# Optimization experiments

Measured on AMD Instinct MI355X. Metric: run time of the kernel, lower is better.

The kernel has to match this reference:

```python
import jax, jax.numpy as jnp
import numpy as np

HID, H, D, DFF = 128, 4, 128, 2048   # hidden_dim, nheads, out_feats per head, dim_feedforward
N, E, B = 32768, 524288, 32
EPS = 1e-5
SLOPE = 0.2  # DGL EdgeGATConv negative_slope default


def setup_inputs() -> dict:
    key = jax.random.key(0)
    ks = jax.random.split(key, 16)
    s = 0.05
    return {
        "h": jax.random.normal(ks[0], (N, HID), jnp.float32),
        "e": jax.random.normal(ks[1], (E, 1), jnp.float32),
        "src": jax.random.randint(ks[2], (E,), 0, N, jnp.int32),
        "dst": jax.random.randint(ks[3], (E,), 0, N, jnp.int32),
        "batch_size": B,
        # EdgeGATConv params (fc / fc_edge / res_fc are bias-free in DGL)
        "W_fc": jax.random.normal(ks[4], (HID, H * D), jnp.float32) * s,
        "attn_l": jax.random.normal(ks[5], (H, D), jnp.float32) * s,
        "attn_r": jax.random.normal(ks[6], (H, D), jnp.float32) * s,
        "W_fe": jax.random.normal(ks[7], (1, H * D), jnp.float32) * s,
        "attn_e": jax.random.normal(ks[8], (H, D), jnp.float32) * s,
        "W_res": jax.random.normal(ks[9], (HID, H * D), jnp.float32) * s,
        "gat_bias": jnp.zeros((H * D,), jnp.float32),
        # linear_mha + norms + FFN
        "W_mha": jax.random.normal(ks[10], (H * D, HID), jnp.float32) * s,
        "b_mha": jnp.zeros((HID,), jnp.float32),
        "n1_g": jnp.ones((HID,), jnp.float32),
        "n1_b": jnp.zeros((HID,), jnp.float32),
        "n2_g": jnp.ones((HID,), jnp.float32),
        "n2_b": jnp.zeros((HID,), jnp.float32),
        "W1": jax.random.normal(ks[11], (HID, DFF), jnp.float32) * s,
        "b1": jnp.zeros((DFF,), jnp.float32),
        "W2": jax.random.normal(ks[12], (DFF, HID), jnp.float32) * s,
        "b2": jnp.zeros((HID,), jnp.float32),
    }


def _ln(x, g, b):
    mu = x.mean(-1, keepdims=True)
    var = ((x - mu) ** 2).mean(-1, keepdims=True)
    return (x - mu) * jax.lax.rsqrt(var + EPS) * g + b


def reference(h, e, src, dst, batch_size, W_fc, attn_l, attn_r, W_fe, attn_e,
              W_res, gat_bias, W_mha, b_mha, n1_g, n1_b, n2_g, n2_b,
              W1, b1, W2, b2):
    n = h.shape[0]
    h0 = h
    # --- EdgeGATConv (eval mode: dropouts are identity) ---
    ft = (h @ W_fc).reshape(n, H, D)                         # (N,H,D)
    el = jnp.einsum("nhd,hd->nh", ft, attn_l)                # (N,H)
    er = jnp.einsum("nhd,hd->nh", ft, attn_r)
    fe = (e @ W_fe).reshape(-1, H, D)                        # (E,H,D)
    ee = jnp.einsum("ehd,hd->eh", fe, attn_e)                # (E,H)
    sc = jax.nn.leaky_relu(el[src] + er[dst] + ee, SLOPE)    # (E,H)
    # segment softmax over incoming edges of each dst node
    m = jax.ops.segment_max(sc, dst, num_segments=n)         # (N,H)
    m = jnp.where(jnp.isfinite(m), m, 0.0)                   # empty segments
    w = jnp.exp(sc - m[dst])
    z = jax.ops.segment_sum(w, dst, num_segments=n)
    zd = z[dst]
    alpha = w / jnp.where(zd == 0, 1.0, zd)                  # (E,H)
    msg = ft[src] * alpha[:, :, None]                        # (E,H,D)
    rst = jax.ops.segment_sum(msg, dst, num_segments=n)      # (N,H,D)
    rst = rst + (h0 @ W_res).reshape(n, H, D) + gat_bias.reshape(1, H, D)
    # --- transformer wrapper ---
    x = jax.nn.relu(rst).reshape(n, H * D)
    x = jax.nn.relu(x @ W_mha + b_mha)
    x = _ln(h0 + x, n1_g, n1_b)
    x = x.reshape(batch_size, -1, x.shape[1])                # (B, N/B, HID)
    ff = jax.nn.relu(x @ W1 + b1) @ W2 + b2
    return _ln(x + ff, n2_g, n2_b)
```

## Files before the change

kernel.cpp:

```cpp
#include <hip/hip_runtime.h>
#include <hip/hip_bf16.h>

#define N_NODES 32768
#define E_EDGES 524288
#define HIDDIM 128
#define FDIM 512
#define DFF 2048
#define LN_EPS 1e-5f
#define SLOPE 0.2f
#define CAP 64

typedef __bf16 bf16_t;
typedef __bf16 bf16x8 __attribute__((ext_vector_type(8)));
typedef float f32x4 __attribute__((ext_vector_type(4)));
typedef float f32x2 __attribute__((ext_vector_type(2)));

#define GLD_LDS16(gp, lp) __builtin_amdgcn_global_load_lds( \
    (const __attribute__((address_space(1))) unsigned int*)(gp), \
    (__attribute__((address_space(3))) unsigned int*)(lp), 16, 0, 0)

__device__ inline unsigned char f32_to_e4m3(float v) {
#if __has_builtin(__builtin_amdgcn_cvt_pk_fp8_f32)
    return (unsigned char)(__builtin_amdgcn_cvt_pk_fp8_f32(v, v, 0, false) & 0xff);
#else
    unsigned bits = __float_as_uint(v);
    unsigned sign = (bits >> 24) & 0x80;
    float av = fabsf(v);
    if (av >= 448.f) return (unsigned char)(sign | 0x7E);
    int e = (int)((bits >> 23) & 0xFF) - 127;
    if (e < -6) { int n = (int)rintf(av * 512.f); return (unsigned char)(sign | n); }
    float ulp = exp2f((float)(e - 3));
    int n = (int)rintf(av / ulp);
    if (n == 16) { e += 1; n = 8; }
    return (unsigned char)(sign | ((e + 7) << 3) | (n - 8));
#endif
}
template<bool HI>
__device__ inline f32x2 e4m3x2_to_f32(unsigned u) {
#if __has_builtin(__builtin_amdgcn_cvt_pk_f32_fp8)
    return __builtin_amdgcn_cvt_pk_f32_fp8(u, HI);
#else
    f32x2 r;
    unsigned b0 = HI ? ((u >> 16) & 0xff) : (u & 0xff);
    unsigned b1 = HI ? ((u >> 24) & 0xff) : ((u >> 8) & 0xff);
    unsigned bs[2] = {b0, b1};
    for (int i = 0; i < 2; ++i) {
        unsigned b = bs[i];
        float s = (b & 0x80) ? -1.f : 1.f;
        int e = (b >> 3) & 15, m = b & 7;
        float v = e ? (8 + m) * exp2f((float)(e - 10)) : m * exp2f(-9.f);
        r[i] = s * v;
    }
    return r;
#endif
}

__device__ inline void pack_range(const float* __restrict__ B, bf16_t* __restrict__ out,
                                  int id, int N) {
    const int g = id / N, n = id % N;
    union { bf16_t b[8]; uint4 u; } pk;
#pragma unroll
    for (int j = 0; j < 8; ++j) pk.b[j] = (bf16_t)B[(size_t)(g * 8 + j) * N + n];
    *(uint4*)(out + (size_t)id * 8) = pk.u;
}

__global__ __launch_bounds__(256) void prep_kernel(const float* __restrict__ h, bf16_t* __restrict__ hb,
                                                   const float* __restrict__ W_fc, bf16_t* __restrict__ Wfc_p,
                                                   const float* __restrict__ W_res, bf16_t* __restrict__ Wres_p,
                                                   const float* __restrict__ W_mha, bf16_t* __restrict__ Wmha_p,
                                                   const float* __restrict__ W1, bf16_t* __restrict__ W1_p,
                                                   const float* __restrict__ W2, bf16_t* __restrict__ W2_p,
                                                   const float* __restrict__ W_fe, const float* __restrict__ attn_e,
                                                   float* __restrict__ ce) {
    int bid = blockIdx.x;
    const int tid = threadIdx.x;
    if (bid < 4096) {
        const int id = bid * 256 + tid;
        const float4 v = ((const float4*)h)[id];
        union { bf16_t b[4]; uint2 u; } pk;
        pk.b[0] = (bf16_t)v.x; pk.b[1] = (bf16_t)v.y; pk.b[2] = (bf16_t)v.z; pk.b[3] = (bf16_t)v.w;
        *(uint2*)(hb + (size_t)id * 4) = pk.u;
        return;
    }
    bid -= 4096;
    if (bid < 32)  { pack_range(W_fc,  Wfc_p,  bid * 256 + tid, 512);  return; }
    bid -= 32;
    if (bid < 32)  { pack_range(W_res, Wres_p, bid * 256 + tid, 512);  return; }
    bid -= 32;
    if (bid < 32)  { pack_range(W_mha, Wmha_p, bid * 256 + tid, 128);  return; }
    bid -= 32;
    if (bid < 128) { pack_range(W1,    W1_p,   bid * 256 + tid, 2048); return; }
    bid -= 128;
    if (bid < 128) { pack_range(W2,    W2_p,   bid * 256 + tid, 128);  return; }
    if (tid < 128) {
        const float4 w = ((const float4*)W_fe)[tid];
        const float4 a = ((const float4*)attn_e)[tid];
        float p = w.x * a.x + w.y * a.y + w.z * a.z + w.w * a.w;
        for (int off = 16; off; off >>= 1) p += __shfl_down(p, off, 32);
        if ((tid & 31) == 0) ce[tid >> 5] = p;
    }
}

__global__ __launch_bounds__(256) void gemm_mfma(const bf16_t* __restrict__ A,
                                                 const bf16_t* __restrict__ Bp,
                                                 bf16_t* __restrict__ C,
                                                 int M, int N, int K) {
    __shared__ __align__(16) bf16_t lA[4096];
    __shared__ __align__(16) bf16_t lB[4096];
    const int tid = threadIdx.x;
    const int lane = tid & 63;
    const int wave = tid >> 6;
    const int wm = (wave >> 1) * 64, wn = (wave & 1) * 64;
    const int row0 = blockIdx.y * 128, col0 = blockIdx.x * 128;
    const int ko = lane >> 4;
    const int rl = lane & 15;
    f32x4 acc[4][4] = {};
    const int c0 = tid, c1 = tid + 256;
    const int g0 = c0 >> 7, m0 = c0 & 127;
    const int g1 = c1 >> 7, m1 = c1 & 127;
    for (int k0 = 0; k0 < K; k0 += 32) {
        __syncthreads();
        GLD_LDS16(A + (size_t)(row0 + m0) * K + k0 + g0 * 8, lA + c0 * 8);
        GLD_LDS16(A + (size_t)(row0 + m1) * K + k0 + g1 * 8, lA + c1 * 8);
        GLD_LDS16(Bp + ((size_t)(k0 / 8 + g0) * N + col0 + m0) * 8, lB + c0 * 8);
        GLD_LDS16(Bp + ((size_t)(k0 / 8 + g1) * N + col0 + m1) * 8, lB + c1 * 8);
        __syncthreads();
        bf16x8 af[4], bfr[4];
#pragma unroll
        for (int i = 0; i < 4; ++i) {
            af[i]  = *(const bf16x8*)&lA[(ko * 128 + wm + i * 16 + rl) * 8];
            bfr[i] = *(const bf16x8*)&lB[(ko * 128 + wn + i * 16 + rl) * 8];
        }
#pragma unroll
        for (int i = 0; i < 4; ++i)
#pragma unroll
            for (int j = 0; j < 4; ++j)
                acc[i][j] = __builtin_amdgcn_mfma_f32_16x16x32_bf16(af[i], bfr[j], acc[i][j], 0, 0, 0);
    }
    const int cr = (lane >> 4) * 4;
    const int cc = lane & 15;
#pragma unroll
    for (int i = 0; i < 4; ++i)
#pragma unroll
        for (int j = 0; j < 4; ++j) {
            const int col = col0 + wn + j * 16 + cc;
#pragma unroll
            for (int r = 0; r < 4; ++r) {
                const int row = row0 + wm + i * 16 + cr + r;
                C[(size_t)row * N + col] = (bf16_t)acc[i][j][r];
            }
        }
}

__global__ __launch_bounds__(256) void gemm_ft(const bf16_t* __restrict__ A,
                                               const bf16_t* __restrict__ Bp,
                                               const float* __restrict__ attn_l,
                                               const float* __restrict__ attn_r,
                                               unsigned char* __restrict__ ft8,
                                               float* __restrict__ el,
                                               float* __restrict__ er) {
    __shared__ __align__(16) bf16_t lA[4096];
    __shared__ __align__(16) bf16_t lB[4096];
    __shared__ float s_el[2][128], s_er[2][128];
    const int tid = threadIdx.x, lane = tid & 63, wave = tid >> 6;
    const int wm = (wave >> 1) * 64, wn = (wave & 1) * 64;
    const int row0 = blockIdx.y * 128;
    const int head = blockIdx.x, col0 = head * 128;
    const int ko = lane >> 4, rl = lane & 15;
    f32x4 acc[4][4] = {};
    const int c0 = tid, c1 = tid + 256;
    const int g0 = c0 >> 7, m0 = c0 & 127;
    const int g1 = c1 >> 7, m1 = c1 & 127;
    for (int k0 = 0; k0 < 128; k0 += 32) {
        __syncthreads();
        GLD_LDS16(A + (size_t)(row0 + m0) * 128 + k0 + g0 * 8, lA + c0 * 8);
        GLD_LDS16(A + (size_t)(row0 + m1) * 128 + k0 + g1 * 8, lA + c1 * 8);
        GLD_LDS16(Bp + ((size_t)(k0 / 8 + g0) * 512 + col0 + m0) * 8, lB + c0 * 8);
        GLD_LDS16(Bp + ((size_t)(k0 / 8 + g1) * 512 + col0 + m1) * 8, lB + c1 * 8);
        __syncthreads();
        bf16x8 af[4], bfr[4];
#pragma unroll
        for (int i = 0; i < 4; ++i) {
            af[i]  = *(const bf16x8*)&lA[(ko * 128 + wm + i * 16 + rl) * 8];
            bfr[i] = *(const bf16x8*)&lB[(ko * 128 + wn + i * 16 + rl) * 8];
        }
#pragma unroll
        for (int i = 0; i < 4; ++i)
#pragma unroll
            for (int j = 0; j < 4; ++j)
                acc[i][j] = __builtin_amdgcn_mfma_f32_16x16x32_bf16(af[i], bfr[j], acc[i][j], 0, 0, 0);
    }
    const int cr = (lane >> 4) * 4, cc = lane & 15;
    float al[4], ar[4];
#pragma unroll
    for (int j = 0; j < 4; ++j) {
        al[j] = attn_l[col0 + wn + j * 16 + cc];
        ar[j] = attn_r[col0 + wn + j * 16 + cc];
    }
#pragma unroll
    for (int i = 0; i < 4; ++i)
#pragma unroll
        for (int r = 0; r < 4; ++r) {
            const int row = row0 + wm + i * 16 + cr + r;
            float pel = 0.f, per = 0.f;
#pragma unroll
            for (int j = 0; j < 4; ++j) {
                const float v = acc[i][j][r];
                ft8[(size_t)row * 512 + col0 + wn + j * 16 + cc] = f32_to_e4m3(v);
                pel += v * al[j];
                per += v * ar[j];
            }
#pragma unroll
            for (int m = 1; m < 16; m <<= 1) {
                pel += __shfl_xor(pel, m);
                per += __shfl_xor(per, m);
            }
            if (cc == 0) {
                s_el[wn >> 6][wm + i * 16 + cr + r] = pel;
                s_er[wn >> 6][wm + i * 16 + cr + r] = per;
            }
        }
    __syncthreads();
    if (tid < 128) {
        el[(size_t)(row0 + tid) * 4 + head] = s_el[0][tid] + s_el[1][tid];
        er[(size_t)(row0 + tid) * 4 + head] = s_er[0][tid] + s_er[1][tid];
    }
}

__global__ __launch_bounds__(256) void gemm_mha_ln(const bf16_t* __restrict__ A,
                                                   const bf16_t* __restrict__ Bp,
                                                   const float* __restrict__ bias,
                                                   const float* __restrict__ h0,
                                                   const float* __restrict__ gamma,
                                                   const float* __restrict__ beta,
                                                   bf16_t* __restrict__ out) {
    __shared__ __align__(16) bf16_t lA[4096];
    __shared__ __align__(16) bf16_t lB[4096];
    __shared__ float s_s1[2][128], s_s2[2][128], s_mu[128], s_rs[128];
    const int tid = threadIdx.x, lane = tid & 63, wave = tid >> 6;
    const int wm = (wave >> 1) * 64, wn = (wave & 1) * 64;
    const int row0 = blockIdx.x * 128;
    const int ko = lane >> 4, rl = lane & 15;
    f32x4 acc[4][4] = {};
    const int c0 = tid, c1 = tid + 256;
    const int g0 = c0 >> 7, m0 = c0 & 127;
    const int g1 = c1 >> 7, m1 = c1 & 127;
    for (int k0 = 0; k0 < 512; k0 += 32) {
        __syncthreads();
        GLD_LDS16(A + (size_t)(row0 + m0) * 512 + k0 + g0 * 8, lA + c0 * 8);
        GLD_LDS16(A + (size_t)(row0 + m1) * 512 + k0 + g1 * 8, lA + c1 * 8);
        GLD_LDS16(Bp + ((size_t)(k0 / 8 + g0) * 128 + m0) * 8, lB + c0 * 8);
        GLD_LDS16(Bp + ((size_t)(k0 / 8 + g1) * 128 + m1) * 8, lB + c1 * 8);
        __syncthreads();
        bf16x8 af[4], bfr[4];
#pragma unroll
        for (int i = 0; i < 4; ++i) {
            af[i]  = *(const bf16x8*)&lA[(ko * 128 + wm + i * 16 + rl) * 8];
            bfr[i] = *(const bf16x8*)&lB[(ko * 128 + wn + i * 16 + rl) * 8];
        }
#pragma unroll
        for (int i = 0; i < 4; ++i)
#pragma unroll
            for (int j = 0; j < 4; ++j)
                acc[i][j] = __builtin_amdgcn_mfma_f32_16x16x32_bf16(af[i], bfr[j], acc[i][j], 0, 0, 0);
    }
    const int cr = (lane >> 4) * 4, cc = lane & 15;
#pragma unroll
    for (int j = 0; j < 4; ++j) {
        const int col = wn + j * 16 + cc;
        const float bb = bias[col];
#pragma unroll
        for (int i = 0; i < 4; ++i)
#pragma unroll
            for (int r = 0; r < 4; ++r) {
                const int row = row0 + wm + i * 16 + cr + r;
                acc[i][j][r] = fmaxf(acc[i][j][r] + bb, 0.f) + h0[(size_t)row * 128 + col];
            }
    }
#pragma unroll
    for (int i = 0; i < 4; ++i)
#pragma unroll
        for (int r = 0; r < 4; ++r) {
            float s1 = 0.f, s2 = 0.f;
#pragma unroll
            for (int j = 0; j < 4; ++j) { const float v = acc[i][j][r]; s1 += v; s2 += v * v; }
#pragma unroll
            for (int m = 1; m < 16; m <<= 1) {
                s1 += __shfl_xor(s1, m);
                s2 += __shfl_xor(s2, m);
            }
            if (cc == 0) {
                s_s1[wn >> 6][wm + i * 16 + cr + r] = s1;
                s_s2[wn >> 6][wm + i * 16 + cr + r] = s2;
            }
        }
    __syncthreads();
    if (tid < 128) {
        const float a = s_s1[0][tid] + s_s1[1][tid];
        const float q = s_s2[0][tid] + s_s2[1][tid];
        const float mu = a * (1.f / 128.f);
        s_mu[tid] = mu;
        s_rs[tid] = rsqrtf(q * (1.f / 128.f) - mu * mu + LN_EPS);
    }
    __syncthreads();
#pragma unroll
    for (int j = 0; j < 4; ++j) {
        const int col = wn + j * 16 + cc;
        const float gg = gamma[col], bb = beta[col];
#pragma unroll
        for (int i = 0; i < 4; ++i)
#pragma unroll
            for (int r = 0; r < 4; ++r) {
                const int rloc = wm + i * 16 + cr + r;
                out[(size_t)(row0 + rloc) * 128 + col] =
                    (bf16_t)((acc[i][j][r] - s_mu[rloc]) * s_rs[rloc] * gg + bb);
            }
    }
}

__global__ __launch_bounds__(512, 1) void ffn_fused(const bf16_t* __restrict__ x3,
                                                    const bf16_t* __restrict__ W1p,
                                                    const float* __restrict__ b1,
                                                    const bf16_t* __restrict__ W2p,
                                                    const float* __restrict__ b2,
                                                    const float* __restrict__ gamma,
                                                    const float* __restrict__ beta,
                                                    float* __restrict__ out) {
    __shared__ __align__(16) bf16_t lW1[8192];
    __shared__ __align__(16) bf16_t lW2[8192];
    __shared__ __align__(16) bf16_t lY[8192];
    __shared__ float s_s1[2][128], s_s2[2][128];
    const int tid = threadIdx.x, lane = tid & 63, wave = tid >> 6;
    const int rg = wave >> 1, cg = wave & 1;
    const int wr = rg * 32;
    const int row0 = blockIdx.x * 128;
    const int ko = lane >> 4, rl = lane & 15;
    const int cr = ko * 4, cc = rl;

#pragma unroll
    for (int it = 0; it < 2; ++it) {
        const int c = it * 512 + tid, g = c >> 6, n = c & 63;
        GLD_LDS16(W1p + ((size_t)g * 2048 + n) * 8, lW1 + c * 8);
    }
    bf16x8 afx[2][4];
#pragma unroll
    for (int i = 0; i < 2; ++i)
#pragma unroll
        for (int kk = 0; kk < 4; ++kk)
            afx[i][kk] = *(const bf16x8*)&x3[(size_t)(row0 + wr + i * 16 + rl) * 128 + (kk * 4 + ko) * 8];

    f32x4 xacc[2][4] = {};
    for (int ch = 0; ch < 32; ++ch) {
        __syncthreads();
#pragma unroll
        for (int it = 0; it < 2; ++it) {
            const int c = it * 512 + tid, g = c >> 7, n = c & 127;
            GLD_LDS16(W2p + ((size_t)(ch * 8 + g) * 128 + n) * 8, lW2 + c * 8);
        }
        f32x4 yacc[2][2] = {};
#pragma unroll
        for (int kk = 0; kk < 4; ++kk) {
            bf16x8 bfr[2];
#pragma unroll
            for (int j = 0; j < 2; ++j)
                bfr[j] = *(const bf16x8*)&lW1[((kk * 4 + ko) * 64 + cg * 32 + j * 16 + rl) * 8];
#pragma unroll
            for (int i = 0; i < 2; ++i)
#pragma unroll
                for (int j = 0; j < 2; ++j)
                    yacc[i][j] = __builtin_amdgcn_mfma_f32_16x16x32_bf16(afx[i][kk], bfr[j], yacc[i][j], 0, 0, 0);
        }
#pragma unroll
        for (int j = 0; j < 2; ++j) {
            const int dff = cg * 32 + j * 16 + cc;
            const float bb = b1[ch * 64 + dff];
#pragma unroll
            for (int i = 0; i < 2; ++i)
#pragma unroll
                for (int r = 0; r < 4; ++r)
                    lY[((dff >> 3) * 128 + wr + i * 16 + cr + r) * 8 + (dff & 7)] =
                        (bf16_t)fmaxf(yacc[i][j][r] + bb, 0.f);
        }
        __syncthreads();
        if (ch + 1 < 32) {
#pragma unroll
            for (int it = 0; it < 2; ++it) {
                const int c = it * 512 + tid, g = c >> 6, n = c & 63;
                GLD_LDS16(W1p + ((size_t)g * 2048 + (ch + 1) * 64 + n) * 8, lW1 + c * 8);
            }
        }
#pragma unroll
        for (int kk = 0; kk < 2; ++kk) {
            bf16x8 afY[2], bfr2[4];
#pragma unroll
            for (int i = 0; i < 2; ++i)
                afY[i] = *(const bf16x8*)&lY[((kk * 4 + ko) * 128 + wr + i * 16 + rl) * 8];
#pragma unroll
            for (int j = 0; j < 4; ++j)
                bfr2[j] = *(const bf16x8*)&lW2[((kk * 4 + ko) * 128 + cg * 64 + j * 16 + rl) * 8];
#pragma unroll
            for (int i = 0; i < 2; ++i)
#pragma unroll
                for (int j = 0; j < 4; ++j)
                    xacc[i][j] = __builtin_amdgcn_mfma_f32_16x16x32_bf16(afY[i], bfr2[j], xacc[i][j], 0, 0, 0);
        }
    }
#pragma unroll
    for (int i = 0; i < 2; ++i)
#pragma unroll
        for (int r = 0; r < 4; ++r) {
            const int row = wr + i * 16 + cr + r;
            float s1 = 0.f, s2 = 0.f;
#pragma unroll
            for (int j = 0; j < 4; ++j) {
                const int col = cg * 64 + j * 16 + cc;
                float v = xacc[i][j][r] + b2[col] + (float)x3[(size_t)(row0 + row) * 128 + col];
                xacc[i][j][r] = v;
                s1 += v; s2 += v * v;
            }
#pragma unroll
            for (int m = 1; m < 16; m <<= 1) {
                s1 += __shfl_xor(s1, m);
                s2 += __shfl_xor(s2, m);
            }
            if (cc == 0) { s_s1[cg][row] = s1; s_s2[cg][row] = s2; }
        }
    __syncthreads();
#pragma unroll
    for (int i = 0; i < 2; ++i)
#pragma unroll
        for (int r = 0; r < 4; ++r) {
            const int row = wr + i * 16 + cr + r;
            const float a = s_s1[0][row] + s_s1[1][row];
            const float q = s_s2[0][row] + s_s2[1][row];
            const float mu = a * (1.f / 128.f);
            const float rs = rsqrtf(q * (1.f / 128.f) - mu * mu + LN_EPS);
#pragma unroll
            for (int j = 0; j < 4; ++j) {
                const int col = cg * 64 + j * 16 + cc;
                out[(size_t)(row0 + row) * 128 + col] =
                    (xacc[i][j][r] - mu) * rs * gamma[col] + beta[col];
            }
        }
}

__global__ __launch_bounds__(256) void edge_build(const float* __restrict__ evals,
                                                  const int* __restrict__ src,
                                                  const int* __restrict__ dst,
                                                  const float* __restrict__ el,
                                                  const float* __restrict__ er,
                                                  const float* __restrict__ ce,
                                                  int* __restrict__ cursor,
                                                  int* __restrict__ csr_src,
                                                  float4* __restrict__ csr_w) {
    const int e = blockIdx.x * 256 + threadIdx.x;
    const int s = src[e], d = dst[e];
    const float ev = evals[e];
    const float4 l = *(const float4*)(el + (size_t)s * 4);
    const float4 r = *(const float4*)(er + (size_t)d * 4);
    const float4 c = *(const float4*)ce;
    float4 w;
    {
        float v;
        v = l.x + r.x + ev * c.x; v = v >= 0.f ? v : SLOPE * v; w.x = __expf(v);
        v = l.y + r.y + ev * c.y; v = v >= 0.f ? v : SLOPE * v; w.y = __expf(v);
        v = l.z + r.z + ev * c.z; v = v >= 0.f ? v : SLOPE * v; w.z = __expf(v);
        v = l.w + r.w + ev * c.w; v = v >= 0.f ? v : SLOPE * v; w.w = __expf(v);
    }
    const int pos = atomicAdd(&cursor[d], 1);
    if (pos < CAP) {
        csr_src[(size_t)d * CAP + pos] = s;
        csr_w[(size_t)d * CAP + pos] = w;
    }
}

__global__ __launch_bounds__(128) void aggregate_kernel(const unsigned char* __restrict__ ft8,
                                                        const bf16_t* __restrict__ res,
                                                        const int* __restrict__ cursor,
                                                        const int* __restrict__ csr_src,
                                                        const float4* __restrict__ csr_w,
                                                        const float* __restrict__ gat_bias,
                                                        bf16_t* __restrict__ x1) {
    const int n = blockIdx.x, t = threadIdx.x;
    __shared__ int s_src[CAP];
    __shared__ float s_w[CAP][4];
    const int deg = min(cursor[n], CAP);
    const int ht = t >> 5;
    if (t < deg) {
        s_src[t] = csr_src[(size_t)n * CAP + t];
        *(float4*)s_w[t] = csr_w[(size_t)n * CAP + t];
    }
    __syncthreads();
    float4 acc = {0.f, 0.f, 0.f, 0.f};
    float z = 0.f;
    for (int j = 0; j < deg; ++j) {
        const float w = s_w[j][ht];
        z += w;
        const unsigned u = *(const unsigned*)(ft8 + (size_t)s_src[j] * 512 + t * 4);
        const f32x2 lo = e4m3x2_to_f32<false>(u);
        const f32x2 hi = e4m3x2_to_f32<true>(u);
        acc.x += w * lo[0]; acc.y += w * lo[1];
        acc.z += w * hi[0]; acc.w += w * hi[1];
    }
    const float rz = deg > 0 ? 1.f / z : 0.f;
    const uint2 ur = *(const uint2*)(res + (size_t)n * FDIM + t * 4);
    const float4 gb = ((const float4*)gat_bias)[t];
    union { bf16_t b[4]; uint2 u; } pk;
    pk.b[0] = (bf16_t)fmaxf(acc.x * rz + __uint_as_float(ur.x << 16) + gb.x, 0.f);
    pk.b[1] = (bf16_t)fmaxf(acc.y * rz + __uint_as_float(ur.x & 0xFFFF0000u) + gb.y, 0.f);
    pk.b[2] = (bf16_t)fmaxf(acc.z * rz + __uint_as_float(ur.y << 16) + gb.z, 0.f);
    pk.b[3] = (bf16_t)fmaxf(acc.w * rz + __uint_as_float(ur.y & 0xFFFF0000u) + gb.w, 0.f);
    *(uint2*)(x1 + (size_t)n * FDIM + t * 4) = pk.u;
}

extern "C" void kernel_launch(void* const* d_in, const int* in_sizes, int n_in,
                              void* d_out, int out_size, void* d_ws, size_t ws_size,
                              hipStream_t stream) {
    const float* h        = (const float*)d_in[0];
    const float* evals    = (const float*)d_in[1];
    const int*   src      = (const int*)d_in[2];
    const int*   dst      = (const int*)d_in[3];
    const float* W_fc     = (const float*)d_in[5];
    const float* attn_l   = (const float*)d_in[6];
    const float* attn_r   = (const float*)d_in[7];
    const float* W_fe     = (const float*)d_in[8];
    const float* attn_e   = (const float*)d_in[9];
    const float* W_res    = (const float*)d_in[10];
    const float* gat_bias = (const float*)d_in[11];
    const float* W_mha    = (const float*)d_in[12];
    const float* b_mha    = (const float*)d_in[13];
    const float* n1_g     = (const float*)d_in[14];
    const float* n1_b     = (const float*)d_in[15];
    const float* n2_g     = (const float*)d_in[16];
    const float* n2_b     = (const float*)d_in[17];
    const float* W1       = (const float*)d_in[18];
    const float* b1       = (const float*)d_in[19];
    const float* W2       = (const float*)d_in[20];
    const float* b2       = (const float*)d_in[21];

    char* ws = (char*)d_ws;
    unsigned char* ft8 = (unsigned char*)(ws + 0);
    bf16_t* res     = (bf16_t*)(ws + 16777216ull);
    bf16_t* x1      = (bf16_t*)(ws + 50331648ull);
    float4* csr_w   = (float4*)(ws + 83886080ull);
    int*    csr_src = (int*)   (ws + 117440512ull);
    bf16_t* x3b     = (bf16_t*)(ws + 125829120ull);
    bf16_t* hb      = (bf16_t*)(ws + 134217728ull);
    bf16_t* Wfc_p   = (bf16_t*)(ws + 142606336ull);
    bf16_t* Wres_p  = (bf16_t*)(ws + 142737408ull);
    bf16_t* Wmha_p  = (bf16_t*)(ws + 142868480ull);
    bf16_t* W1_p    = (bf16_t*)(ws + 142999552ull);
    bf16_t* W2_p    = (bf16_t*)(ws + 143523840ull);
    float*  el      = (float*) (ws + 144048128ull);
    float*  er      = (float*) (ws + 144572416ull);
    float*  ce      = (float*) (ws + 145096704ull);
    int*    cursor  = (int*)   (ws + 145096768ull);

    if (ws_size < 146000000ull) return;

    (void)hipMemsetAsync(cursor, 0, 131072, stream);

    prep_kernel<<<4449, 256, 0, stream>>>(h, hb, W_fc, Wfc_p, W_res, Wres_p,
                                          W_mha, Wmha_p, W1, W1_p, W2, W2_p,
                                          W_fe, attn_e, ce);
    gemm_ft<<<dim3(4, 256), 256, 0, stream>>>(hb, Wfc_p, attn_l, attn_r, ft8, el, er);
    gemm_mfma<<<dim3(4, 256), 256, 0, stream>>>(hb, Wres_p, res, N_NODES, FDIM, 128);
    edge_build<<<E_EDGES / 256, 256, 0, stream>>>(evals, src, dst, el, er, ce, cursor, csr_src, csr_w);
    aggregate_kernel<<<N_NODES, 128, 0, stream>>>(ft8, res, cursor, csr_src, csr_w, gat_bias, x1);
    gemm_mha_ln<<<256, 256, 0, stream>>>(x1, Wmha_p, b_mha, h, n1_g, n1_b, x3b);
    ffn_fused<<<256, 512, 0, stream>>>(x3b, W1_p, b1, W2_p, b2, n2_g, n2_b, (float*)d_out);
}
```

Baseline: 300.2 us.

## Store edge weights as bf16, fold cursor reset into prep, pack two nodes per block

Edge softmax weights are now stored as packed bf16 (8 bytes per edge instead of 16), which halves the CSR weight traffic written by edge_build and read by aggregate. The separate memset of the cursor array is dropped and the zeroing is done by extra blocks in prep_kernel, removing one launch. The aggregate kernel now handles two destination nodes per 256-thread block, halving the block count. The risks are lower precision in the attention weights and the normaliser computed from them.

```diff
diff --git a/kernel.cpp b/kernel.cpp
--- a/kernel.cpp
+++ b/kernel.cpp
@@ -71,7 +71,7 @@
                                                    const float* __restrict__ W1, bf16_t* __restrict__ W1_p,
                                                    const float* __restrict__ W2, bf16_t* __restrict__ W2_p,
                                                    const float* __restrict__ W_fe, const float* __restrict__ attn_e,
-                                                   float* __restrict__ ce) {
+                                                   float* __restrict__ ce, int* __restrict__ cursor) {
     int bid = blockIdx.x;
     const int tid = threadIdx.x;
     if (bid < 4096) {
@@ -92,6 +92,8 @@
     if (bid < 128) { pack_range(W1,    W1_p,   bid * 256 + tid, 2048); return; }
     bid -= 128;
     if (bid < 128) { pack_range(W2,    W2_p,   bid * 256 + tid, 128);  return; }
+    bid -= 128;
+    if (bid < 128) { cursor[bid * 256 + tid] = 0; return; }
     if (tid < 128) {
         const float4 w = ((const float4*)W_fe)[tid];
         const float4 a = ((const float4*)attn_e)[tid];
@@ -452,65 +454,71 @@
                                                   const float* __restrict__ ce,
                                                   int* __restrict__ cursor,
                                                   int* __restrict__ csr_src,
-                                                  float4* __restrict__ csr_w) {
+                                                  uint2* __restrict__ csr_w) {
     const int e = blockIdx.x * 256 + threadIdx.x;
     const int s = src[e], d = dst[e];
     const float ev = evals[e];
     const float4 l = *(const float4*)(el + (size_t)s * 4);
     const float4 r = *(const float4*)(er + (size_t)d * 4);
     const float4 c = *(const float4*)ce;
-    float4 w;
+    union { bf16_t b[4]; uint2 u; } pw;
     {
         float v;
-        v = l.x + r.x + ev * c.x; v = v >= 0.f ? v : SLOPE * v; w.x = __expf(v);
-        v = l.y + r.y + ev * c.y; v = v >= 0.f ? v : SLOPE * v; w.y = __expf(v);
-        v = l.z + r.z + ev * c.z; v = v >= 0.f ? v : SLOPE * v; w.z = __expf(v);
-        v = l.w + r.w + ev * c.w; v = v >= 0.f ? v : SLOPE * v; w.w = __expf(v);
+        v = l.x + r.x + ev * c.x; v = v >= 0.f ? v : SLOPE * v; pw.b[0] = (bf16_t)__expf(v);
+        v = l.y + r.y + ev * c.y; v = v >= 0.f ? v : SLOPE * v; pw.b[1] = (bf16_t)__expf(v);
+        v = l.z + r.z + ev * c.z; v = v >= 0.f ? v : SLOPE * v; pw.b[2] = (bf16_t)__expf(v);
+        v = l.w + r.w + ev * c.w; v = v >= 0.f ? v : SLOPE * v; pw.b[3] = (bf16_t)__expf(v);
     }
     const int pos = atomicAdd(&cursor[d], 1);
     if (pos < CAP) {
         csr_src[(size_t)d * CAP + pos] = s;
-        csr_w[(size_t)d * CAP + pos] = w;
-    }
-}
-
-__global__ __launch_bounds__(128) void aggregate_kernel(const unsigned char* __restrict__ ft8,
+        csr_w[(size_t)d * CAP + pos] = pw.u;
+    }
+}
+
+__global__ __launch_bounds__(256) void aggregate_kernel(const unsigned char* __restrict__ ft8,
                                                         const bf16_t* __restrict__ res,
                                                         const int* __restrict__ cursor,
                                                         const int* __restrict__ csr_src,
-                                                        const float4* __restrict__ csr_w,
+                                                        const uint2* __restrict__ csr_w,
                                                         const float* __restrict__ gat_bias,
                                                         bf16_t* __restrict__ x1) {
-    const int n = blockIdx.x, t = threadIdx.x;
-    __shared__ int s_src[CAP];
-    __shared__ float s_w[CAP][4];
+    const int t = threadIdx.x;
+    const int which = t >> 7, lt = t & 127;
+    const int n = blockIdx.x * 2 + which;
+    __shared__ int s_src[2][CAP];
+    __shared__ float s_w[2][CAP][4];
     const int deg = min(cursor[n], CAP);
-    const int ht = t >> 5;
-    if (t < deg) {
-        s_src[t] = csr_src[(size_t)n * CAP + t];
-        *(float4*)s_w[t] = csr_w[(size_t)n * CAP + t];
+    const int ht = lt >> 5;
+    if (lt < CAP && lt < deg) {
+        s_src[which][lt] = csr_src[(size_t)n * CAP + lt];
+        const uint2 wu = csr_w[(size_t)n * CAP + lt];
+        s_w[which][lt][0] = __uint_as_float(wu.x << 16);
+        s_w[which][lt][1] = __uint_as_float(wu.x & 0xFFFF0000u);
+        s_w[which][lt][2] = __uint_as_float(wu.y << 16);
+        s_w[which][lt][3] = __uint_as_float(wu.y & 0xFFFF0000u);
     }
     __syncthreads();
     float4 acc = {0.f, 0.f, 0.f, 0.f};
     float z = 0.f;
     for (int j = 0; j < deg; ++j) {
-        const float w = s_w[j][ht];
+        const float w = s_w[which][j][ht];
         z += w;
-        const unsigned u = *(const unsigned*)(ft8 + (size_t)s_src[j] * 512 + t * 4);
+        const unsigned u = *(const unsigned*)(ft8 + (size_t)s_src[which][j] * 512 + lt * 4);
         const f32x2 lo = e4m3x2_to_f32<false>(u);
         const f32x2 hi = e4m3x2_to_f32<true>(u);
         acc.x += w * lo[0]; acc.y += w * lo[1];
         acc.z += w * hi[0]; acc.w += w * hi[1];
     }
     const float rz = deg > 0 ? 1.f / z : 0.f;
-    const uint2 ur = *(const uint2*)(res + (size_t)n * FDIM + t * 4);
-    const float4 gb = ((const float4*)gat_bias)[t];
+    const uint2 ur = *(const uint2*)(res + (size_t)n * FDIM + lt * 4);
+    const float4 gb = ((const float4*)gat_bias)[lt];
     union { bf16_t b[4]; uint2 u; } pk;
     pk.b[0] = (bf16_t)fmaxf(acc.x * rz + __uint_as_float(ur.x << 16) + gb.x, 0.f);
     pk.b[1] = (bf16_t)fmaxf(acc.y * rz + __uint_as_float(ur.x & 0xFFFF0000u) + gb.y, 0.f);
     pk.b[2] = (bf16_t)fmaxf(acc.z * rz + __uint_as_float(ur.y << 16) + gb.z, 0.f);
     pk.b[3] = (bf16_t)fmaxf(acc.w * rz + __uint_as_float(ur.y & 0xFFFF0000u) + gb.w, 0.f);
-    *(uint2*)(x1 + (size_t)n * FDIM + t * 4) = pk.u;
+    *(uint2*)(x1 + (size_t)n * FDIM + lt * 4) = pk.u;
 }
 
 extern "C" void kernel_launch(void* const* d_in, const int* in_sizes, int n_in,
@@ -542,31 +550,29 @@
     unsigned char* ft8 = (unsigned char*)(ws + 0);
     bf16_t* res     = (bf16_t*)(ws + 16777216ull);
     bf16_t* x1      = (bf16_t*)(ws + 50331648ull);
-    float4* csr_w   = (float4*)(ws + 83886080ull);
-    int*    csr_src = (int*)   (ws + 117440512ull);
-    bf16_t* x3b     = (bf16_t*)(ws + 125829120ull);
-    bf16_t* hb      = (bf16_t*)(ws + 134217728ull);
-    bf16_t* Wfc_p   = (bf16_t*)(ws + 142606336ull);
-    bf16_t* Wres_p  = (bf16_t*)(ws + 142737408ull);
-    bf16_t* Wmha_p  = (bf16_t*)(ws + 142868480ull);
-    bf16_t* W1_p    = (bf16_t*)(ws + 142999552ull);
-    bf16_t* W2_p    = (bf16_t*)(ws + 143523840ull);
-    float*  el      = (float*) (ws + 144048128ull);
-    float*  er      = (float*) (ws + 144572416ull);
-    float*  ce      = (float*) (ws + 145096704ull);
-    int*    cursor  = (int*)   (ws + 145096768ull);
-
-    if (ws_size < 146000000ull) return;
-
-    (void)hipMemsetAsync(cursor, 0, 131072, stream);
-
-    prep_kernel<<<4449, 256, 0, stream>>>(h, hb, W_fc, Wfc_p, W_res, Wres_p,
+    uint2*  csr_w   = (uint2*) (ws + 83886080ull);
+    int*    csr_src = (int*)   (ws + 100663296ull);
+    bf16_t* x3b     = (bf16_t*)(ws + 109051904ull);
+    bf16_t* hb      = (bf16_t*)(ws + 117440512ull);
+    bf16_t* Wfc_p   = (bf16_t*)(ws + 125829120ull);
+    bf16_t* Wres_p  = (bf16_t*)(ws + 125960192ull);
+    bf16_t* Wmha_p  = (bf16_t*)(ws + 126091264ull);
+    bf16_t* W1_p    = (bf16_t*)(ws + 126222336ull);
+    bf16_t* W2_p    = (bf16_t*)(ws + 126746624ull);
+    float*  el      = (float*) (ws + 127270912ull);
+    float*  er      = (float*) (ws + 127795200ull);
+    float*  ce      = (float*) (ws + 128319488ull);
+    int*    cursor  = (int*)   (ws + 128319552ull);
+
+    if (ws_size < 128500000ull) return;
+
+    prep_kernel<<<4577, 256, 0, stream>>>(h, hb, W_fc, Wfc_p, W_res, Wres_p,
                                           W_mha, Wmha_p, W1, W1_p, W2, W2_p,
-                                          W_fe, attn_e, ce);
+                                          W_fe, attn_e, ce, cursor);
     gemm_ft<<<dim3(4, 256), 256, 0, stream>>>(hb, Wfc_p, attn_l, attn_r, ft8, el, er);
     gemm_mfma<<<dim3(4, 256), 256, 0, stream>>>(hb, Wres_p, res, N_NODES, FDIM, 128);
     edge_build<<<E_EDGES / 256, 256, 0, stream>>>(evals, src, dst, el, er, ce, cursor, csr_src, csr_w);
-    aggregate_kernel<<<N_NODES, 128, 0, stream>>>(ft8, res, cursor, csr_src, csr_w, gat_bias, x1);
+    aggregate_kernel<<<N_NODES / 2, 256, 0, stream>>>(ft8, res, cursor, csr_src, csr_w, gat_bias, x1);
     gemm_mha_ln<<<256, 256, 0, stream>>>(x1, Wmha_p, b_mha, h, n1_g, n1_b, x3b);
     ffn_fused<<<256, 512, 0, stream>>>(x3b, W1_p, b1, W2_p, b2, n2_g, n2_b, (float*)d_out);
 }
```

After: 310.1 us. 3.3% more time.
